# Performance work log

Hardware: AMD Instinct MI355X
Metric: run time of the kernel (lower is better)

Reference implementation:

```python
import jax, jax.numpy as jnp
import numpy as np

E, N, D, H = 16, 2048, 1024, 4096

def setup_inputs() -> dict:
    key = jax.random.key(0)
    k1, k2, k3 = jax.random.split(key, 3)
    x = jax.random.normal(k1, (E, N, D), dtype=jnp.float32)
    # init_tensor in the repo is Kaiming-style uniform init; use uniform(-1/sqrt(fan_in), 1/sqrt(fan_in))
    s1 = 1.0 / np.sqrt(D)
    s2 = 1.0 / np.sqrt(H)
    w1 = jax.random.uniform(k2, (E, D, H), dtype=jnp.float32, minval=-s1, maxval=s1)
    w2 = jax.random.uniform(k3, (E, H, D), dtype=jnp.float32, minval=-s2, maxval=s2)
    return {"x": x, "w1": w1, "w2": w2}

def reference(x, w1, w2):
    # per-expert 2-layer MLP: grouped GEMM -> GELU -> grouped GEMM
    hidden = jnp.einsum('end,edh->enh', x, w1)
    hidden = jax.nn.gelu(hidden, approximate=False)  # torch nn.GELU default (erf)
    out = jnp.einsum('enh,ehd->end', hidden, w2)
    return out
```

## Files before the change

### kernel.cpp

```cpp
#include <hip/hip_runtime.h>
#include <stdint.h>
#include <math.h>

#define E_    16
#define NTOK  2048
#define D_    1024
#define H_    4096

typedef unsigned short ushort_t;
typedef __attribute__((ext_vector_type(8))) short short8;
typedef __attribute__((ext_vector_type(4))) float f32x4;

__device__ __forceinline__ ushort_t f2bf(float f) {
    union { float f; unsigned int u; } v; v.f = f;
    unsigned int u = v.u;
    return (ushort_t)((u + 0x7FFFu + ((u >> 16) & 1u)) >> 16);
}

__device__ __forceinline__ void async_copy16(const ushort_t* g, ushort_t* l) {
    __builtin_amdgcn_global_load_lds(
        (const __attribute__((address_space(1))) void*)g,
        (__attribute__((address_space(3))) void*)l,
        16, 0, 0);
}


__global__ void cvt_f32_bf16(const float* __restrict__ in, ushort_t* __restrict__ out) {
    int i = blockIdx.x * blockDim.x + threadIdx.x;
    const float4 v = *(const float4*)(in + (size_t)i * 4);
    ushort4 o;
    o.x = f2bf(v.x); o.y = f2bf(v.y); o.z = f2bf(v.z); o.w = f2bf(v.w);
    *(ushort4*)(out + (size_t)i * 4) = o;
}

__global__ void transpose_cvt(const float* __restrict__ in, ushort_t* __restrict__ out,
                              int R, int C) {
    __shared__ float tile[64][65];
    const int e = blockIdx.z;
    const float*  inp  = in  + (size_t)e * R * C;
    ushort_t*     outp = out + (size_t)e * R * C;
    const int c0 = blockIdx.x * 64, r0 = blockIdx.y * 64;
    const int tx = threadIdx.x & 15, ty = threadIdx.x >> 4;
    #pragma unroll
    for (int i = 0; i < 4; ++i) {
        const int r = i * 16 + ty;
        const float4 v = *(const float4*)(inp + (size_t)(r0 + r) * C + c0 + tx * 4);
        tile[r][tx * 4 + 0] = v.x; tile[r][tx * 4 + 1] = v.y;
        tile[r][tx * 4 + 2] = v.z; tile[r][tx * 4 + 3] = v.w;
    }
    __syncthreads();
    #pragma unroll
    for (int i = 0; i < 4; ++i) {
        const int c = i * 16 + ty;
        ushort4 o;
        o.x = f2bf(tile[tx * 4 + 0][c]); o.y = f2bf(tile[tx * 4 + 1][c]);
        o.z = f2bf(tile[tx * 4 + 2][c]); o.w = f2bf(tile[tx * 4 + 3][c]);
        *(ushort4*)(outp + (size_t)(c0 + c) * R + r0 + tx * 4) = o;
    }
}


template<bool GELU, typename CT>
__global__ void gemm_bt(const ushort_t* __restrict__ A, const ushort_t* __restrict__ Bt,
                        CT* __restrict__ C, int M, int N, int K) {
    constexpr int SMEM_USH = GELU ? (128 * 130) : (128 * 64 * 2);
    __shared__ ushort_t smem[SMEM_USH];
    ushort_t* As = smem;
    ushort_t* Bs = smem + 128 * 64;

    const int e  = blockIdx.z;
    const int bm = blockIdx.y, bn = blockIdx.x;
    const ushort_t* Ae = A  + (size_t)e * M * K + (size_t)(bm * 128) * K;
    const ushort_t* Be = Bt + (size_t)e * N * K + (size_t)(bn * 128) * K;
    CT* Ce = C + (size_t)e * M * N;

    const int tid  = threadIdx.x;
    const int wave = tid >> 6, lane = tid & 63;
    const int wm = wave & 1, wn = wave >> 1;
    const int lr = lane & 15;
    const int h  = lr & 7;
    const int cq = lane >> 4;

    f32x4 acc[4][4];
    #pragma unroll
    for (int i = 0; i < 4; ++i)
        #pragma unroll
        for (int j = 0; j < 4; ++j)
            acc[i][j] = (f32x4)(0.0f);

    const int row_s = lane >> 3;
    const int ch    = ((lane & 7) ^ row_s) * 8;

    const int KT = K >> 6;
    for (int kt = 0; kt < KT; ++kt) {
        const int k0 = kt * 64;
        #pragma unroll
        for (int t = 0; t < 4; ++t) {
            const int rb = (wave * 4 + t) * 8;
            async_copy16(Ae + (size_t)(rb + row_s) * K + k0 + ch, &As[rb * 64]);
            async_copy16(Be + (size_t)(rb + row_s) * K + k0 + ch, &Bs[rb * 64]);
        }
        __syncthreads();

        #pragma unroll
        for (int kk = 0; kk < 2; ++kk) {
            short8 a[4], b[4];
            #pragma unroll
            for (int i = 0; i < 4; ++i)
                a[i] = *(const short8*)&As[(wm * 64 + i * 16 + lr) * 64 +
                                           (((kk * 4 + cq) ^ h) << 3)];
            #pragma unroll
            for (int j = 0; j < 4; ++j)
                b[j] = *(const short8*)&Bs[(wn * 64 + j * 16 + lr) * 64 +
                                           (((kk * 4 + cq) ^ h) << 3)];
            #pragma unroll
            for (int i = 0; i < 4; ++i)
                #pragma unroll
                for (int j = 0; j < 4; ++j)
                    acc[i][j] = __builtin_amdgcn_mfma_f32_16x16x32_bf16(
                        a[i], b[j], acc[i][j], 0, 0, 0);
        }
        __syncthreads();
    }

    const int cr = (lane >> 4) * 4;
    const int cc = lane & 15;

    if constexpr (GELU) {
        #pragma unroll
        for (int i = 0; i < 4; ++i)
            #pragma unroll
            for (int j = 0; j < 4; ++j)
                #pragma unroll
                for (int r = 0; r < 4; ++r) {
                    const int row = wm * 64 + i * 16 + cr + r;
                    const int col = wn * 64 + j * 16 + cc;
                    float v = acc[i][j][r];
                    v = 0.5f * v * (1.0f + erff(v * 0.70710678118654752f));
                    smem[row * 130 + col] = f2bf(v);
                }
        __syncthreads();
        const unsigned int* p32 = (const unsigned int*)smem;
        const int rty = tid >> 4, rtx = tid & 15;
        #pragma unroll
        for (int it = 0; it < 8; ++it) {
            const int row = it * 16 + rty;
            const int base = row * 65 + rtx * 4;
            uint4 v;
            v.x = p32[base + 0]; v.y = p32[base + 1];
            v.z = p32[base + 2]; v.w = p32[base + 3];
            *(uint4*)(Ce + (size_t)(bm * 128 + row) * N + bn * 128 + rtx * 8) = v;
        }
    } else {
        #pragma unroll
        for (int i = 0; i < 4; ++i)
            #pragma unroll
            for (int j = 0; j < 4; ++j)
                #pragma unroll
                for (int r = 0; r < 4; ++r) {
                    const int row = bm * 128 + wm * 64 + i * 16 + cr + r;
                    const int col = bn * 128 + wn * 64 + j * 16 + cc;
                    Ce[(size_t)row * N + col] = acc[i][j][r];
                }
    }
}


extern "C" void kernel_launch(void* const* d_in, const int* in_sizes, int n_in,
                              void* d_out, int out_size, void* d_ws, size_t ws_size,
                              hipStream_t stream) {
    const float* x  = (const float*)d_in[0];
    const float* w1 = (const float*)d_in[1];
    const float* w2 = (const float*)d_in[2];
    float* out = (float*)d_out;

    ushort_t* xb  = (ushort_t*)d_ws;
    ushort_t* w1t = xb  + (size_t)E_ * NTOK * D_;
    ushort_t* w2t = w1t + (size_t)E_ * D_ * H_;
    ushort_t* hid = w2t + (size_t)E_ * H_ * D_;

    {
        const size_t n = (size_t)E_ * NTOK * D_;
        cvt_f32_bf16<<<dim3((unsigned)(n / 4 / 256)), dim3(256), 0, stream>>>(x, xb);
    }
    transpose_cvt<<<dim3(H_ / 64, D_ / 64, E_), dim3(256), 0, stream>>>(w1, w1t, D_, H_);
    transpose_cvt<<<dim3(D_ / 64, H_ / 64, E_), dim3(256), 0, stream>>>(w2, w2t, H_, D_);

    gemm_bt<true, ushort_t><<<dim3(H_ / 128, NTOK / 128, E_), dim3(256), 0, stream>>>(
        xb, w1t, hid, NTOK, H_, D_);

    gemm_bt<false, float><<<dim3(D_ / 128, NTOK / 128, E_), dim3(256), 0, stream>>>(
        hid, w2t, out, NTOK, D_, H_);
}
```

Measured before the change: 1.294 ms.

## Rewrite grouped GEMM as 256x256 tile kernel with 4-stage async LDS pipeline

Replaces the 128x128 single-buffered bf16 GEMM with a 512-thread, 256x256-tile kernel. It uses a 4-stage global_load_lds pipeline with explicit vmcnt waits, split-phase MFMA scheduling with s_setprio, and XCD-aware workgroup remapping. The larger tiles raise reuse per LDS load, and the multi-stage prefetch hides global latency behind compute. The cost is heavy register use (128 accumulator floats per lane), a 128KB LDS footprint that limits occupancy, and hand-written barrier/waitcnt ordering that could break correctness if miscounted.

After: 1.285 ms. About the same (-0.6%).

```diff
diff --git a/kernel.cpp b/kernel.cpp
--- a/kernel.cpp
+++ b/kernel.cpp
@@ -17,7 +17,7 @@
     return (ushort_t)((u + 0x7FFFu + ((u >> 16) & 1u)) >> 16);
 }
 
-__device__ __forceinline__ void async_copy16(const ushort_t* g, ushort_t* l) {
+__device__ __forceinline__ void async_copy16(const void* g, ushort_t* l) {
     __builtin_amdgcn_global_load_lds(
         (const __attribute__((address_space(1))) void*)g,
         (__attribute__((address_space(3))) void*)l,
@@ -60,107 +60,153 @@
 }
 
 
+#define BARR()  { asm volatile("" ::: "memory"); __builtin_amdgcn_s_barrier(); \
+                  asm volatile("" ::: "memory"); }
+#define LGKM0() { asm volatile("s_waitcnt lgkmcnt(0)" ::: "memory"); \
+                  __builtin_amdgcn_sched_barrier(0); }
+#define VMC(n)  { asm volatile("s_waitcnt vmcnt(" #n ")" ::: "memory"); }
+
+#define SA(s, off) { async_copy16(ag0 + (off), aL0 + (s) * 8192); \
+                     async_copy16(ag1 + (off), aL1 + (s) * 8192); }
+#define SB(s, off) { async_copy16(bg0 + (off), bL0 + (s) * 8192); \
+                     async_copy16(bg1 + (off), bL1 + (s) * 8192); }
+
+#define LDA(s, m) (*(const short8*)&lds[aFB + (s) * 8192 + (m) * 512])
+#define LDB(s, n) (*(const short8*)&lds[bFB + (s) * 8192 + (n) * 512])
+#define MM(m, n, va, vb) acc[m][n] = __builtin_amdgcn_mfma_f32_16x16x32_bf16(va, vb, acc[m][n], 0, 0, 0)
+
+#define PH_A(s, STG) { \
+    a0 = LDA(s, 0); a1 = LDA(s, 1); a2 = LDA(s, 2); a3 = LDA(s, 3); \
+    b0 = LDB(s, 0); b1 = LDB(s, 1); b2 = LDB(s, 2); b3 = LDB(s, 3); \
+    STG; BARR(); LGKM0(); \
+    __builtin_amdgcn_s_setprio(1); \
+    MM(0,0,a0,b0); MM(0,1,a0,b1); MM(0,2,a0,b2); MM(0,3,a0,b3); \
+    MM(1,0,a1,b0); MM(1,1,a1,b1); MM(1,2,a1,b2); MM(1,3,a1,b3); \
+    MM(2,0,a2,b0); MM(2,1,a2,b1); MM(2,2,a2,b2); MM(2,3,a2,b3); \
+    MM(3,0,a3,b0); MM(3,1,a3,b1); MM(3,2,a3,b2); MM(3,3,a3,b3); \
+    __builtin_amdgcn_s_setprio(0); BARR(); }
+
+#define PH_B(s, STG) { \
+    a0 = LDA(s, 4); a1 = LDA(s, 5); a2 = LDA(s, 6); a3 = LDA(s, 7); \
+    STG; BARR(); LGKM0(); \
+    __builtin_amdgcn_s_setprio(1); \
+    MM(4,0,a0,b0); MM(4,1,a0,b1); MM(4,2,a0,b2); MM(4,3,a0,b3); \
+    MM(5,0,a1,b0); MM(5,1,a1,b1); MM(5,2,a1,b2); MM(5,3,a1,b3); \
+    MM(6,0,a2,b0); MM(6,1,a2,b1); MM(6,2,a2,b2); MM(6,3,a2,b3); \
+    MM(7,0,a3,b0); MM(7,1,a3,b1); MM(7,2,a3,b2); MM(7,3,a3,b3); \
+    __builtin_amdgcn_s_setprio(0); BARR(); }
+
 template<bool GELU, typename CT>
-__global__ void gemm_bt(const ushort_t* __restrict__ A, const ushort_t* __restrict__ Bt,
-                        CT* __restrict__ C, int M, int N, int K) {
-    constexpr int SMEM_USH = GELU ? (128 * 130) : (128 * 64 * 2);
-    __shared__ ushort_t smem[SMEM_USH];
-    ushort_t* As = smem;
-    ushort_t* Bs = smem + 128 * 64;
-
-    const int e  = blockIdx.z;
-    const int bm = blockIdx.y, bn = blockIdx.x;
-    const ushort_t* Ae = A  + (size_t)e * M * K + (size_t)(bm * 128) * K;
-    const ushort_t* Be = Bt + (size_t)e * N * K + (size_t)(bn * 128) * K;
-    CT* Ce = C + (size_t)e * M * N;
+__global__ __launch_bounds__(512, 2)
+void gemm256(const ushort_t* __restrict__ A, const ushort_t* __restrict__ Bt,
+             CT* __restrict__ C, int M, int N, int K, int tn, int per_e) {
+    __shared__ __align__(16) ushort_t lds[65536];
+
+    int wg = blockIdx.x;
+    const int cpx = (int)gridDim.x >> 3;
+    wg = (wg & 7) * cpx + (wg >> 3);
+    const int e  = wg / per_e;
+    const int r2 = wg - e * per_e;
+    const int bm = r2 / tn;
+    const int bn = r2 - bm * tn;
 
     const int tid  = threadIdx.x;
     const int wave = tid >> 6, lane = tid & 63;
-    const int wm = wave & 1, wn = wave >> 1;
-    const int lr = lane & 15;
-    const int h  = lr & 7;
-    const int cq = lane >> 4;
-
-    f32x4 acc[4][4];
+    const int wm = wave >> 2, wn = wave & 3;
+    const int lr = lane & 15, cq = lane >> 4;
+    const int lh = lr >> 1, lp = lr & 1;
+    const int fsw = ((((lp << 2) | cq) ^ lh) << 3);
+    const int aFB = (wm * 64 + lh) * 64 + fsw;
+    const int bFB = 32768 + (wn * 32 + lh) * 64 + fsw;
+
+    const int l8  = lane >> 3;
+    const int lc  = (lane & 7) ^ l8;
+    const int par = lc >> 2, cch = lc & 3;
+
+    const size_t K2 = (size_t)K * 2;
+    const ushort_t* Ae = A  + (size_t)e * M * K + (size_t)(bm * 256) * K;
+    const ushort_t* Be = Bt + (size_t)e * N * K + (size_t)(bn * 256) * K;
+    CT* Ce = C + (size_t)e * M * N;
+
+    const char* ag0 = (const char*)Ae + (size_t)(16 * wave + 2 * l8 + par) * K2 + cch * 16;
+    const char* ag1 = ag0 + 128 * K2;
+    const char* bg0 = (const char*)Be + (size_t)(16 * wave + 2 * l8 + par) * K2 + cch * 16;
+    const char* bg1 = bg0 + 128 * K2;
+    ushort_t* aL0 = &lds[wave * 512];
+    ushort_t* aL1 = &lds[(8 + wave) * 512];
+    ushort_t* bL0 = &lds[32768 + wave * 512];
+    ushort_t* bL1 = &lds[32768 + (8 + wave) * 512];
+
+    f32x4 acc[8][4];
     #pragma unroll
-    for (int i = 0; i < 4; ++i)
-        #pragma unroll
-        for (int j = 0; j < 4; ++j)
-            acc[i][j] = (f32x4)(0.0f);
-
-    const int row_s = lane >> 3;
-    const int ch    = ((lane & 7) ^ row_s) * 8;
-
-    const int KT = K >> 6;
-    for (int kt = 0; kt < KT; ++kt) {
-        const int k0 = kt * 64;
-        #pragma unroll
-        for (int t = 0; t < 4; ++t) {
-            const int rb = (wave * 4 + t) * 8;
-            async_copy16(Ae + (size_t)(rb + row_s) * K + k0 + ch, &As[rb * 64]);
-            async_copy16(Be + (size_t)(rb + row_s) * K + k0 + ch, &Bs[rb * 64]);
-        }
-        __syncthreads();
-
-        #pragma unroll
-        for (int kk = 0; kk < 2; ++kk) {
-            short8 a[4], b[4];
+    for (int i = 0; i < 8; ++i)
+        #pragma unroll
+        for (int j = 0; j < 4; ++j) acc[i][j] = (f32x4)(0.0f);
+
+    short8 a0, a1, a2, a3, b0, b1, b2, b3;
+
+    SB(0, 0); SA(0, 0); SB(1, 64); SA(1, 64); SB(2, 128); SA(2, 128); SB(3, 192);
+    VMC(6);
+    BARR();
+
+    const int T = K >> 7;
+    for (int t = 0; t < T - 1; ++t) {
+        PH_A(0, SA(3, 192));
+        PH_B(0, SB(0, 256));
+        PH_A(1, SA(0, 256));
+        PH_B(1, VMC(4); SB(1, 320));
+        PH_A(2, SA(1, 320));
+        PH_B(2, SB(2, 384));
+        PH_A(3, SA(2, 384));
+        PH_B(3, VMC(4); SB(3, 448));
+        ag0 += 256; ag1 += 256; bg0 += 256; bg1 += 256;
+    }
+    PH_A(0, SA(3, 192));
+    PH_B(0, (void)0);
+    PH_A(1, (void)0);
+    PH_B(1, VMC(0));
+    PH_A(2, (void)0);
+    PH_B(2, (void)0);
+    PH_A(3, (void)0);
+    PH_B(3, (void)0);
+
+    const int crow = (lane >> 4) * 4;
+    const int ccol = lane & 15;
+    if constexpr (GELU) {
+        #pragma unroll
+        for (int m = 0; m < 8; ++m) {
+            const int rowb = wm * 128 + m * 16 + crow;
             #pragma unroll
-            for (int i = 0; i < 4; ++i)
-                a[i] = *(const short8*)&As[(wm * 64 + i * 16 + lr) * 64 +
-                                           (((kk * 4 + cq) ^ h) << 3)];
-            #pragma unroll
-            for (int j = 0; j < 4; ++j)
-                b[j] = *(const short8*)&Bs[(wn * 64 + j * 16 + lr) * 64 +
-                                           (((kk * 4 + cq) ^ h) << 3)];
-            #pragma unroll
-            for (int i = 0; i < 4; ++i)
-                #pragma unroll
-                for (int j = 0; j < 4; ++j)
-                    acc[i][j] = __builtin_amdgcn_mfma_f32_16x16x32_bf16(
-                        a[i], b[j], acc[i][j], 0, 0, 0);
-        }
-        __syncthreads();
-    }
-
-    const int cr = (lane >> 4) * 4;
-    const int cc = lane & 15;
-
-    if constexpr (GELU) {
-        #pragma unroll
-        for (int i = 0; i < 4; ++i)
-            #pragma unroll
-            for (int j = 0; j < 4; ++j)
+            for (int n = 0; n < 4; ++n) {
+                const int col = wn * 64 + n * 16 + ccol;
                 #pragma unroll
                 for (int r = 0; r < 4; ++r) {
-                    const int row = wm * 64 + i * 16 + cr + r;
-                    const int col = wn * 64 + j * 16 + cc;
-                    float v = acc[i][j][r];
+                    const int rw = rowb + r;
+                    float v = acc[m][n][r];
                     v = 0.5f * v * (1.0f + erff(v * 0.70710678118654752f));
-                    smem[row * 130 + col] = f2bf(v);
+                    lds[rw * 256 + ((((col >> 3) ^ (rw & 31)) << 3) | (col & 7))] = f2bf(v);
                 }
-        __syncthreads();
-        const unsigned int* p32 = (const unsigned int*)smem;
-        const int rty = tid >> 4, rtx = tid & 15;
-        #pragma unroll
-        for (int it = 0; it < 8; ++it) {
-            const int row = it * 16 + rty;
-            const int base = row * 65 + rtx * 4;
-            uint4 v;
-            v.x = p32[base + 0]; v.y = p32[base + 1];
-            v.z = p32[base + 2]; v.w = p32[base + 3];
-            *(uint4*)(Ce + (size_t)(bm * 128 + row) * N + bn * 128 + rtx * 8) = v;
+            }
+        }
+        asm volatile("s_waitcnt lgkmcnt(0)" ::: "memory");
+        __builtin_amdgcn_s_barrier();
+        #pragma unroll
+        for (int it = 0; it < 16; ++it) {
+            const int row = it * 16 + (tid >> 5);
+            const int g8 = tid & 31;
+            short8 v = *(const short8*)&lds[row * 256 + ((g8 ^ (row & 31)) << 3)];
+            *(short8*)((ushort_t*)Ce + (size_t)(bm * 256 + row) * N + bn * 256 + g8 * 8) = v;
         }
     } else {
         #pragma unroll
-        for (int i = 0; i < 4; ++i)
+        for (int m = 0; m < 8; ++m)
             #pragma unroll
-            for (int j = 0; j < 4; ++j)
+            for (int n = 0; n < 4; ++n)
                 #pragma unroll
                 for (int r = 0; r < 4; ++r) {
-                    const int row = bm * 128 + wm * 64 + i * 16 + cr + r;
-                    const int col = bn * 128 + wn * 64 + j * 16 + cc;
-                    Ce[(size_t)row * N + col] = acc[i][j][r];
+                    const int row = bm * 256 + wm * 128 + m * 16 + crow + r;
+                    const int col = bn * 256 + wn * 64 + n * 16 + ccol;
+                    Ce[(size_t)row * N + col] = acc[m][n][r];
                 }
     }
 }
@@ -186,9 +232,9 @@
     transpose_cvt<<<dim3(H_ / 64, D_ / 64, E_), dim3(256), 0, stream>>>(w1, w1t, D_, H_);
     transpose_cvt<<<dim3(D_ / 64, H_ / 64, E_), dim3(256), 0, stream>>>(w2, w2t, H_, D_);
 
-    gemm_bt<true, ushort_t><<<dim3(H_ / 128, NTOK / 128, E_), dim3(256), 0, stream>>>(
-        xb, w1t, hid, NTOK, H_, D_);
-
-    gemm_bt<false, float><<<dim3(D_ / 128, NTOK / 128, E_), dim3(256), 0, stream>>>(
-        hid, w2t, out, NTOK, D_, H_);
-}
+    gemm256<true, ushort_t><<<dim3(2048), dim3(512), 0, stream>>>(
+        xb, w1t, hid, NTOK, H_, D_, 16, 128);
+
+    gemm256<false, float><<<dim3(512), dim3(512), 0, stream>>>(
+        hid, w2t, out, NTOK, D_, H_, 4, 32);
+}
```
